# Performance work log

Hardware: AMD Instinct MI355X
Metric: run time of the kernel (lower is better)

The kernel has to match this reference:

```python
import jax, jax.numpy as jnp
import numpy as np

BN_EPS = 1e-5

def setup_inputs() -> dict:
    key = jax.random.key(0)
    k1, k2 = jax.random.split(key)
    B, C, H, W, K = 256, 2048, 7, 7, 16
    featmap = jax.random.normal(k1, (B, C, H, W), dtype=jnp.float32)
    w16 = jax.random.normal(k2, (K, C), dtype=jnp.float32) * 0.02  # 1x1 conv weight
    bn_gamma = jnp.ones((K,), jnp.float32)
    bn_beta = jnp.zeros((K,), jnp.float32)
    bn_mean = jnp.zeros((K,), jnp.float32)
    bn_var = jnp.ones((K,), jnp.float32)
    return {"featmap": featmap, "w16": w16, "bn_gamma": bn_gamma,
            "bn_beta": bn_beta, "bn_mean": bn_mean, "bn_var": bn_var}

def reference(featmap, w16, bn_gamma, bn_beta, bn_mean, bn_var):
    # featmap: [B, 2048, 7, 7]; 1x1 conv -> featcov16: [B, 16, 7, 7]
    featcov16 = jnp.einsum('bchw,kc->bkhw', featmap, w16)
    # BatchNorm2d(16), inference-style with running stats
    inv = bn_gamma / jnp.sqrt(bn_var + BN_EPS)
    featcov16 = featcov16 * inv[None, :, None, None] + (bn_beta - bn_mean * inv)[None, :, None, None]
    # Loop-free bilinear pooling: original repeats featcov16[:,i] to 2048 ch,
    # multiplies with featmap, and AvgPool2d(7) -> mean over HxW.
    HW = featmap.shape[2] * featmap.shape[3]
    feat_matrix = jnp.einsum('bkhw,bchw->bkc', featcov16, featmap) / HW  # [B,16,2048]
    bp_out_feat = feat_matrix.reshape(feat_matrix.shape[0], -1)  # [B, 32768]
    return bp_out_feat
```

## Files before the change

### kernel.cpp

```cpp
#include <hip/hip_runtime.h>

#define BATCH 256
#define CDIM  2048
#define HW    49
#define KDIM  16

#define OSTRIP 8
#define SC     256
#define STRIP_B (SC * HW * 4)

#define GLDS(g, l) __builtin_amdgcn_global_load_lds(                        \
        (const __attribute__((address_space(1))) unsigned int*)(g),          \
        (__attribute__((address_space(3))) unsigned int*)(l), 16, 0, 0)


__global__ __launch_bounds__(256) void prep_kernel(
    const float* __restrict__ w16,
    const float* __restrict__ gamma, const float* __restrict__ beta,
    const float* __restrict__ mean,  const float* __restrict__ var,
    float* __restrict__ wT, float* __restrict__ pscr)
{
    const int idx = blockIdx.x * 256 + threadIdx.x;
    const int c = idx >> 4, k = idx & 15;
    const float inv = gamma[k] * rsqrtf(var[k] + 1e-5f) * (1.0f / 49.0f);
    wT[idx] = w16[k * CDIM + c] * inv;

    for (int i = idx; i < BATCH * (HW * KDIM); i += 128 * 256) {
        const int kk = i & 15;
        const float invk = gamma[kk] * rsqrtf(var[kk] + 1e-5f);
        pscr[i] = (beta[kk] - mean[kk] * invk) * (1.0f / 49.0f);
    }
}

__global__ __launch_bounds__(256) void conv_kernel(
    const float* __restrict__ fm, const float* __restrict__ wT,
    float* __restrict__ pscr)
{
    __shared__ __align__(16) float fbuf[SC * HW + 4];

    const int tid  = threadIdx.x;
    const int b    = blockIdx.x >> 3;
    const int o    = blockIdx.x & 7;
    const int wavu = __builtin_amdgcn_readfirstlane(tid >> 6);
    const int lane = tid & 63;
    const int hwi  = lane < HW ? lane : HW - 1;

    {
        const char* gbase = (const char*)fm
            + (size_t)b * (CDIM * HW * 4) + (size_t)o * STRIP_B;
        char* lbase = (char*)fbuf;
        const int nld = (wavu == 0) ? 13 : 12;
        for (int i = 0; i < nld; ++i) {
            const int j = wavu + 4 * i;
            GLDS(gbase + j * 1024 + lane * 16, lbase + j * 1024);
        }
    }
    __syncthreads();

    float acc[KDIM];
    #pragma unroll
    for (int k = 0; k < KDIM; ++k) acc[k] = 0.f;

    const int cl0 = wavu * 64;
    const float4* __restrict__ wq = (const float4*)(wT + (size_t)((o * SC + cl0) << 4));

    #pragma unroll 8
    for (int cc = 0; cc < 64; ++cc) {
        const float fv = fbuf[(cl0 + cc) * HW + hwi];
        const float4 w0 = wq[cc * 4 + 0];
        const float4 w1 = wq[cc * 4 + 1];
        const float4 w2 = wq[cc * 4 + 2];
        const float4 w3 = wq[cc * 4 + 3];
        acc[0]  += w0.x * fv; acc[1]  += w0.y * fv; acc[2]  += w0.z * fv; acc[3]  += w0.w * fv;
        acc[4]  += w1.x * fv; acc[5]  += w1.y * fv; acc[6]  += w1.z * fv; acc[7]  += w1.w * fv;
        acc[8]  += w2.x * fv; acc[9]  += w2.y * fv; acc[10] += w2.z * fv; acc[11] += w2.w * fv;
        acc[12] += w3.x * fv; acc[13] += w3.y * fv; acc[14] += w3.z * fv; acc[15] += w3.w * fv;
    }

    __syncthreads();
    float* red = fbuf;
    if (lane < HW) {
        #pragma unroll
        for (int k = 0; k < KDIM; ++k)
            red[wavu * (KDIM * 52) + k * 52 + lane] = acc[k];
    }
    __syncthreads();

    for (int p = tid; p < HW * KDIM; p += 256) {
        const int k = p / HW, hw = p - k * HW;
        const int a = k * 52 + hw;
        const float s = red[a] + red[a + 832] + red[a + 1664] + red[a + 2496];
        atomicAdd(&pscr[(size_t)b * 784 + hw * KDIM + k], s);
    }
}

__global__ __launch_bounds__(256) void bp_kernel(
    const float* __restrict__ fm, const float* __restrict__ pscr,
    float* __restrict__ out)
{
    __shared__ __align__(16) float fs[SC * HW];

    const int tid  = threadIdx.x;
    const int b    = blockIdx.x >> 3;
    const int oc   = (blockIdx.x & 7) * SC;
    const int wavu = __builtin_amdgcn_readfirstlane(tid >> 6);
    const int lane = tid & 63;

    {
        const char* gbase = (const char*)fm + ((size_t)b * CDIM + oc) * (HW * 4);
        char* lbase = (char*)fs;
        const int nld = (wavu == 0) ? 13 : 12;
        for (int i = 0; i < nld; ++i) {
            const int j = wavu + 4 * i;
            GLDS(gbase + j * 1024 + lane * 16, lbase + j * 1024);
        }
    }
    __syncthreads();

    const float4* __restrict__ P4 = (const float4*)(pscr + (size_t)b * 784);

    float acc[KDIM];
    #pragma unroll
    for (int k = 0; k < KDIM; ++k) acc[k] = 0.f;

    const float* row = fs + tid * HW;
    #pragma unroll
    for (int hw = 0; hw < HW; ++hw) {
        const float fv = row[hw];
        const float4 p0 = P4[hw * 4 + 0];
        const float4 p1 = P4[hw * 4 + 1];
        const float4 p2 = P4[hw * 4 + 2];
        const float4 p3 = P4[hw * 4 + 3];
        acc[0]  += p0.x * fv; acc[1]  += p0.y * fv; acc[2]  += p0.z * fv; acc[3]  += p0.w * fv;
        acc[4]  += p1.x * fv; acc[5]  += p1.y * fv; acc[6]  += p1.z * fv; acc[7]  += p1.w * fv;
        acc[8]  += p2.x * fv; acc[9]  += p2.y * fv; acc[10] += p2.z * fv; acc[11] += p2.w * fv;
        acc[12] += p3.x * fv; acc[13] += p3.y * fv; acc[14] += p3.z * fv; acc[15] += p3.w * fv;
    }

    float* ob = out + (size_t)b * (KDIM * CDIM) + oc + tid;
    #pragma unroll
    for (int k = 0; k < KDIM; ++k) ob[k * CDIM] = acc[k];
}

extern "C" void kernel_launch(void* const* d_in, const int* in_sizes, int n_in,
                              void* d_out, int out_size, void* d_ws, size_t ws_size,
                              hipStream_t stream) {
    const float* fm    = (const float*)d_in[0];
    const float* w16   = (const float*)d_in[1];
    const float* gamma = (const float*)d_in[2];
    const float* beta  = (const float*)d_in[3];
    const float* mean  = (const float*)d_in[4];
    const float* var   = (const float*)d_in[5];
    float* out  = (float*)d_out;
    float* wT   = (float*)d_ws;
    float* pscr = (float*)d_ws + CDIM * KDIM;

    prep_kernel<<<128, 256, 0, stream>>>(w16, gamma, beta, mean, var, wT, pscr);
    conv_kernel<<<BATCH * OSTRIP, 256, 0, stream>>>(fm, wT, pscr);
    bp_kernel<<<BATCH * OSTRIP, 256, 0, stream>>>(fm, pscr, out);
}
```

Baseline: 250.3 us.

## Process whole batch per block with double-buffered LDS chunk pipeline

```diff
diff --git a/kernel.cpp b/kernel.cpp
--- a/kernel.cpp
+++ b/kernel.cpp
@@ -5,141 +5,178 @@
 #define HW    49
 #define KDIM  16
 
-#define OSTRIP 8
-#define SC     256
-#define STRIP_B (SC * HW * 4)
+#define NCHUNK  8
+#define CC      256
+#define CHUNK_B (CC * HW * 4)
+#define CHUNK_F (CC * HW)
 
 #define GLDS(g, l) __builtin_amdgcn_global_load_lds(                        \
         (const __attribute__((address_space(1))) unsigned int*)(g),          \
         (__attribute__((address_space(3))) unsigned int*)(l), 16, 0, 0)
+#define WAITVM(N) do { asm volatile("s_waitcnt vmcnt(" #N ")" ::: "memory"); \
+                       __builtin_amdgcn_sched_barrier(0); } while (0)
+#define SBAR()    __builtin_amdgcn_s_barrier()
 
 
 __global__ __launch_bounds__(256) void prep_kernel(
     const float* __restrict__ w16,
-    const float* __restrict__ gamma, const float* __restrict__ beta,
-    const float* __restrict__ mean,  const float* __restrict__ var,
-    float* __restrict__ wT, float* __restrict__ pscr)
+    const float* __restrict__ gamma, const float* __restrict__ var,
+    float* __restrict__ wT)
 {
     const int idx = blockIdx.x * 256 + threadIdx.x;
     const int c = idx >> 4, k = idx & 15;
     const float inv = gamma[k] * rsqrtf(var[k] + 1e-5f) * (1.0f / 49.0f);
     wT[idx] = w16[k * CDIM + c] * inv;
-
-    for (int i = idx; i < BATCH * (HW * KDIM); i += 128 * 256) {
-        const int kk = i & 15;
-        const float invk = gamma[kk] * rsqrtf(var[kk] + 1e-5f);
-        pscr[i] = (beta[kk] - mean[kk] * invk) * (1.0f / 49.0f);
-    }
 }
 
-__global__ __launch_bounds__(256) void conv_kernel(
+__global__ __launch_bounds__(512) void conv_kernel(
     const float* __restrict__ fm, const float* __restrict__ wT,
+    const float* __restrict__ gamma, const float* __restrict__ beta,
+    const float* __restrict__ mean,  const float* __restrict__ var,
     float* __restrict__ pscr)
 {
-    __shared__ __align__(16) float fbuf[SC * HW + 4];
+    __shared__ __align__(16) float buf0[CHUNK_F];
+    __shared__ __align__(16) float buf1[CHUNK_F];
+    __shared__ __align__(16) float red[8 * KDIM * 52];
 
     const int tid  = threadIdx.x;
-    const int b    = blockIdx.x >> 3;
-    const int o    = blockIdx.x & 7;
+    const int b    = blockIdx.x;
     const int wavu = __builtin_amdgcn_readfirstlane(tid >> 6);
     const int lane = tid & 63;
     const int hwi  = lane < HW ? lane : HW - 1;
 
-    {
-        const char* gbase = (const char*)fm
-            + (size_t)b * (CDIM * HW * 4) + (size_t)o * STRIP_B;
-        char* lbase = (char*)fbuf;
-        const int nld = (wavu == 0) ? 13 : 12;
-        for (int i = 0; i < nld; ++i) {
-            const int j = wavu + 4 * i;
-            GLDS(gbase + j * 1024 + lane * 16, lbase + j * 1024);
+    const char* gb = (const char*)fm + (size_t)b * (CDIM * HW * 4);
+
+    if (wavu < 7) {
+        #pragma unroll
+        for (int i = 0; i < 7; ++i) {
+            const int j = wavu * 7 + i;
+            GLDS(gb + j * 1024 + lane * 16, (char*)buf0 + j * 1024);
         }
     }
-    __syncthreads();
 
     float acc[KDIM];
     #pragma unroll
     for (int k = 0; k < KDIM; ++k) acc[k] = 0.f;
 
-    const int cl0 = wavu * 64;
-    const float4* __restrict__ wq = (const float4*)(wT + (size_t)((o * SC + cl0) << 4));
+    for (int t = 0; t < NCHUNK; ++t) {
+        float* cur = (t & 1) ? buf1 : buf0;
+        float* nxt = (t & 1) ? buf0 : buf1;
 
-    #pragma unroll 8
-    for (int cc = 0; cc < 64; ++cc) {
-        const float fv = fbuf[(cl0 + cc) * HW + hwi];
-        const float4 w0 = wq[cc * 4 + 0];
-        const float4 w1 = wq[cc * 4 + 1];
-        const float4 w2 = wq[cc * 4 + 2];
-        const float4 w3 = wq[cc * 4 + 3];
-        acc[0]  += w0.x * fv; acc[1]  += w0.y * fv; acc[2]  += w0.z * fv; acc[3]  += w0.w * fv;
-        acc[4]  += w1.x * fv; acc[5]  += w1.y * fv; acc[6]  += w1.z * fv; acc[7]  += w1.w * fv;
-        acc[8]  += w2.x * fv; acc[9]  += w2.y * fv; acc[10] += w2.z * fv; acc[11] += w2.w * fv;
-        acc[12] += w3.x * fv; acc[13] += w3.y * fv; acc[14] += w3.z * fv; acc[15] += w3.w * fv;
+        if (t < NCHUNK - 1) {
+            if (wavu < 7) {
+                #pragma unroll
+                for (int i = 0; i < 7; ++i) {
+                    const int j = wavu * 7 + i;
+                    GLDS(gb + (size_t)(t + 1) * CHUNK_B + j * 1024 + lane * 16,
+                         (char*)nxt + j * 1024);
+                }
+            }
+            WAITVM(7);
+        } else {
+            WAITVM(0);
+        }
+        SBAR();
+
+        const float4* __restrict__ wq =
+            (const float4*)(wT + (size_t)((t * CC + wavu * 32) << 4));
+        #pragma unroll 8
+        for (int cc = 0; cc < 32; ++cc) {
+            const float fv = cur[(wavu * 32 + cc) * HW + hwi];
+            const float4 w0 = wq[cc * 4 + 0];
+            const float4 w1 = wq[cc * 4 + 1];
+            const float4 w2 = wq[cc * 4 + 2];
+            const float4 w3 = wq[cc * 4 + 3];
+            acc[0]  += w0.x * fv; acc[1]  += w0.y * fv; acc[2]  += w0.z * fv; acc[3]  += w0.w * fv;
+            acc[4]  += w1.x * fv; acc[5]  += w1.y * fv; acc[6]  += w1.z * fv; acc[7]  += w1.w * fv;
+            acc[8]  += w2.x * fv; acc[9]  += w2.y * fv; acc[10] += w2.z * fv; acc[11] += w2.w * fv;
+            acc[12] += w3.x * fv; acc[13] += w3.y * fv; acc[14] += w3.z * fv; acc[15] += w3.w * fv;
+        }
+        SBAR();
     }
 
-    __syncthreads();
-    float* red = fbuf;
     if (lane < HW) {
         #pragma unroll
         for (int k = 0; k < KDIM; ++k)
             red[wavu * (KDIM * 52) + k * 52 + lane] = acc[k];
     }
     __syncthreads();
-
-    for (int p = tid; p < HW * KDIM; p += 256) {
-        const int k = p / HW, hw = p - k * HW;
+    for (int p = tid; p < HW * KDIM; p += 512) {
+        const int k = p & 15, hw = p >> 4;
         const int a = k * 52 + hw;
-        const float s = red[a] + red[a + 832] + red[a + 1664] + red[a + 2496];
-        atomicAdd(&pscr[(size_t)b * 784 + hw * KDIM + k], s);
+        float s = 0.f;
+        #pragma unroll
+        for (int w = 0; w < 8; ++w) s += red[w * 832 + a];
+        const float inv = gamma[k] * rsqrtf(var[k] + 1e-5f);
+        pscr[(size_t)b * 784 + p] = s + (beta[k] - mean[k] * inv) * (1.0f / 49.0f);
     }
 }
 
-__global__ __launch_bounds__(256) void bp_kernel(
+__global__ __launch_bounds__(512) void bp_kernel(
     const float* __restrict__ fm, const float* __restrict__ pscr,
     float* __restrict__ out)
 {
-    __shared__ __align__(16) float fs[SC * HW];
+    __shared__ __align__(16) float buf0[CHUNK_F];
+    __shared__ __align__(16) float buf1[CHUNK_F];
+    __shared__ __align__(16) float pad[3 * 256];
 
     const int tid  = threadIdx.x;
-    const int b    = blockIdx.x >> 3;
-    const int oc   = (blockIdx.x & 7) * SC;
+    const int b    = blockIdx.x;
     const int wavu = __builtin_amdgcn_readfirstlane(tid >> 6);
     const int lane = tid & 63;
+    const bool dma = (wavu >= 4);
+    const int  w4  = wavu - 4;
 
-    {
-        const char* gbase = (const char*)fm + ((size_t)b * CDIM + oc) * (HW * 4);
-        char* lbase = (char*)fs;
-        const int nld = (wavu == 0) ? 13 : 12;
-        for (int i = 0; i < nld; ++i) {
-            const int j = wavu + 4 * i;
-            GLDS(gbase + j * 1024 + lane * 16, lbase + j * 1024);
-        }
-    }
-    __syncthreads();
+    const char* gb = (const char*)fm + (size_t)b * (CDIM * HW * 4);
+
+#define BP_ISSUE(T, DSTBUF) do {                                             \
+        _Pragma("unroll")                                                    \
+        for (int i = 0; i < 13; ++i) {                                       \
+            const int j  = w4 * 13 + i;                           \
+            const int jj = j < 49 ? j : 48;                                  \
+            char* dst = (j < 49) ? (char*)(DSTBUF) + j * 1024                \
+                                 : (char*)pad + (j - 49) * 1024;             \
+            GLDS(gb + (size_t)(T) * CHUNK_B + jj * 1024 + lane * 16, dst);   \
+        } } while (0)
+
+    if (dma) BP_ISSUE(0, buf0);
 
     const float4* __restrict__ P4 = (const float4*)(pscr + (size_t)b * 784);
 
-    float acc[KDIM];
-    #pragma unroll
-    for (int k = 0; k < KDIM; ++k) acc[k] = 0.f;
+    for (int t = 0; t < NCHUNK; ++t) {
+        float* cur = (t & 1) ? buf1 : buf0;
+        float* nxt = (t & 1) ? buf0 : buf1;
 
-    const float* row = fs + tid * HW;
-    #pragma unroll
-    for (int hw = 0; hw < HW; ++hw) {
-        const float fv = row[hw];
-        const float4 p0 = P4[hw * 4 + 0];
-        const float4 p1 = P4[hw * 4 + 1];
-        const float4 p2 = P4[hw * 4 + 2];
-        const float4 p3 = P4[hw * 4 + 3];
-        acc[0]  += p0.x * fv; acc[1]  += p0.y * fv; acc[2]  += p0.z * fv; acc[3]  += p0.w * fv;
-        acc[4]  += p1.x * fv; acc[5]  += p1.y * fv; acc[6]  += p1.z * fv; acc[7]  += p1.w * fv;
-        acc[8]  += p2.x * fv; acc[9]  += p2.y * fv; acc[10] += p2.z * fv; acc[11] += p2.w * fv;
-        acc[12] += p3.x * fv; acc[13] += p3.y * fv; acc[14] += p3.z * fv; acc[15] += p3.w * fv;
+        if (dma) {
+            if (t < NCHUNK - 1) { BP_ISSUE(t + 1, nxt); WAITVM(13); }
+            else                { WAITVM(0); }
+        }
+        SBAR();
+
+        if (!dma) {
+            float a[KDIM];
+            #pragma unroll
+            for (int k = 0; k < KDIM; ++k) a[k] = 0.f;
+            const float* row = cur + tid * HW;
+            #pragma unroll
+            for (int hw = 0; hw < HW; ++hw) {
+                const float fv = row[hw];
+                const float4 p0 = P4[hw * 4 + 0];
+                const float4 p1 = P4[hw * 4 + 1];
+                const float4 p2 = P4[hw * 4 + 2];
+                const float4 p3 = P4[hw * 4 + 3];
+                a[0]  += p0.x * fv; a[1]  += p0.y * fv; a[2]  += p0.z * fv; a[3]  += p0.w * fv;
+                a[4]  += p1.x * fv; a[5]  += p1.y * fv; a[6]  += p1.z * fv; a[7]  += p1.w * fv;
+                a[8]  += p2.x * fv; a[9]  += p2.y * fv; a[10] += p2.z * fv; a[11] += p2.w * fv;
+                a[12] += p3.x * fv; a[13] += p3.y * fv; a[14] += p3.z * fv; a[15] += p3.w * fv;
+            }
+            float* ob = out + (size_t)b * (KDIM * CDIM) + t * CC + tid;
+            #pragma unroll
+            for (int k = 0; k < KDIM; ++k) ob[k * CDIM] = a[k];
+        }
+        SBAR();
     }
-
-    float* ob = out + (size_t)b * (KDIM * CDIM) + oc + tid;
-    #pragma unroll
-    for (int k = 0; k < KDIM; ++k) ob[k * CDIM] = acc[k];
+#undef BP_ISSUE
 }
 
 extern "C" void kernel_launch(void* const* d_in, const int* in_sizes, int n_in,
@@ -155,7 +192,7 @@
     float* wT   = (float*)d_ws;
     float* pscr = (float*)d_ws + CDIM * KDIM;
 
-    prep_kernel<<<128, 256, 0, stream>>>(w16, gamma, beta, mean, var, wT, pscr);
-    conv_kernel<<<BATCH * OSTRIP, 256, 0, stream>>>(fm, wT, pscr);
-    bp_kernel<<<BATCH * OSTRIP, 256, 0, stream>>>(fm, pscr, out);
+    prep_kernel<<<128, 256, 0, stream>>>(w16, gamma, var, wT);
+    conv_kernel<<<BATCH, 512, 0, stream>>>(fm, wT, gamma, beta, mean, var, pscr);
+    bp_kernel<<<BATCH, 512, 0, stream>>>(fm, pscr, out);
 }
```

Measured after the change: 268.6 us. +7.3%, slower.
